# Optimization experiments

Measured on AMD Instinct MI355X. Metric: run time of the kernel, lower is better.

The kernel has to match this reference:

```python
import jax, jax.numpy as jnp
import numpy as np
import math


def hs_pe(x, fr, fi):
    # x: [N, c, h, w], c = cp*3; fr/fi: [max_len, cp] real/imag of freqs_cis.
    N, c, h, w = x.shape
    cp = c // 3
    xs = x.reshape(N, cp, 3, h, w)
    a, b, c3 = xs[:, :, 0], xs[:, :, 1], xs[:, :, 2]
    # rotate (a, b) as complex along h axis
    frh = fr[:h].T[None, :, :, None]  # [1, cp, h, 1]
    fih = fi[:h].T[None, :, :, None]
    a2 = a * frh - b * fih
    b2 = a * fih + b * frh
    # rotate (b2, c3) as complex along w axis
    frw = fr[:w].T[None, :, None, :]  # [1, cp, 1, w]
    fiw = fi[:w].T[None, :, None, :]
    b3 = b2 * frw - c3 * fiw
    c32 = b2 * fiw + c3 * frw
    return jnp.stack([a2, b3, c32], axis=2).reshape(N, c, h, w)


def partition(x, ws, dr):
    # OverlapDilatedWindowPartion
    B, C, H, W = x.shape
    Wsz = ws + dr
    st = Wsz // 2
    nh = math.ceil(H / Wsz)
    nw = math.ceil(W / Wsz)
    x = jnp.pad(x, ((0, 0), (0, 0), (0, nh * Wsz - H), (0, nw * Wsz - W)), mode='reflect')
    x = jnp.concatenate([x, jnp.pad(x[:, :, st:, :], ((0, 0), (0, 0), (0, st), (0, 0)), mode='reflect')], axis=0)
    x = jnp.concatenate([x, jnp.pad(x[:, :, :, st:], ((0, 0), (0, 0), (0, 0), (0, st)), mode='reflect')], axis=0)
    gb = x.shape[0]
    # 'gb c (nh h) (nw w) -> (nh nw gb) c h w'
    x = x.reshape(gb, C, nh, Wsz, nw, Wsz).transpose(2, 4, 0, 1, 3, 5).reshape(nh * nw * gb, C, Wsz, Wsz)
    return x[:, :, :ws, :ws]


def reverse(win, ws, dr, B, H, W):
    # OverlapDilatedWindowReverse
    Wsz = ws + dr
    st = Wsz // 2
    nh = math.ceil(H / Wsz)
    nw = math.ceil(W / Wsz)
    bH, bW = nh * Wsz, nw * Wsz
    win = jnp.pad(win, ((0, 0), (0, 0), (0, dr), (0, dr)))
    C = win.shape[1]
    # '(nh nw g b) c h w -> g b c (nh h) (nw w)'
    x = win.reshape(nh, nw, 4, B, C, Wsz, Wsz).transpose(2, 3, 4, 0, 5, 1, 6).reshape(4, B, C, bH, bW)
    x0 = x[0]
    x1 = jnp.pad(x[1], ((0, 0), (0, 0), (st, 0), (0, 0)))[:, :, :bH, :]
    x2 = jnp.pad(x[2], ((0, 0), (0, 0), (0, 0), (st, 0)))[:, :, :, :bW]
    x3 = jnp.pad(x[3], ((0, 0), (0, 0), (st, 0), (st, 0)))[:, :, :bH, :bW]
    return (x0 + x1 + x2 + x3)[:, :, :H, :W]


HEAD_NUM = 8
WINDOW_SIZE = 8
DILATE_RATE = 4


def setup_inputs() -> dict:
    key = jax.random.key(0)
    k1, k2, k3 = jax.random.split(key, 3)
    B, C, H, W = 1, 576, 192, 192
    x = jax.random.normal(k1, (B, C, H, W), dtype=jnp.float32)
    # rotary frequencies on the unit circle: [window_size, d//3, 2] (real, imag)
    theta = jax.random.uniform(k2, (WINDOW_SIZE, C // (3 * HEAD_NUM) // 3), dtype=jnp.float32) * (2 * np.pi)
    freqs_cis = jnp.stack([jnp.cos(theta), jnp.sin(theta)], axis=-1)
    weight = jax.random.uniform(k3, (1, 1, H, W), dtype=jnp.float32, minval=0.5, maxval=1.5)
    return {"x": x, "freqs_cis": freqs_cis, "weight": weight}


def reference(x, freqs_cis, weight):
    B, C, H, W = x.shape
    ws, dr, n = WINDOW_SIZE, DILATE_RATE, HEAD_NUM
    win = partition(x, ws, dr)  # [Nw, C, ws, ws]
    Nw = win.shape[0]
    d = C // (3 * n)
    # '(k n d)' channel split, k outer, d fastest
    qkv = win.reshape(Nw, 3, n, d, ws, ws).transpose(1, 0, 2, 3, 4, 5).reshape(3, Nw * n, d, ws, ws)
    fr, fi = freqs_cis[..., 0], freqs_cis[..., 1]
    q = hs_pe(qkv[0], fr, fi)
    k = hs_pe(qkv[1], fr, fi)
    v = qkv[2]
    def toseq(t):
        return t.reshape(Nw * n, d, ws * ws).transpose(0, 2, 1)  # [Nw*n, L, d]
    q, k, v = toseq(q), toseq(k), toseq(v)
    scale = jnp.sqrt(jnp.asarray(d, q.dtype))
    attn = jax.nn.softmax(jnp.einsum('nld,nmd->nlm', q, k) / scale, axis=-1)
    out = jnp.einsum('nlm,nmd->nld', attn, v)
    # '(Nw n) (h w) d -> Nw (n d) h w'
    out = out.reshape(Nw, n, ws, ws, d).transpose(0, 1, 4, 2, 3).reshape(Nw, n * d, ws, ws)
    out = reverse(out, ws, dr, B, H, W)
    return out / weight
```

## Files before the change

### kernel.cpp

```cpp
#include <hip/hip_runtime.h>

#define HW 36864
#define HDIM 192
#define NUNITS 8192
#define UPB 2
#define UDW 2688
#define QO 0
#define KO 768
#define VTO 1536
#define PO 0
#define O_BYTES (8192ull * 768 * 4)
#define Y_BYTES (8ull * HW * 72 * 2)

typedef __fp16 h2  __attribute__((ext_vector_type(2)));
typedef __fp16 v8h __attribute__((ext_vector_type(8)));
typedef float  v4f __attribute__((ext_vector_type(4)));

static __device__ __forceinline__ h2 pk2(float a, float b) {
    return __builtin_amdgcn_cvt_pkrtz(a, b);
}
static __device__ __forceinline__ unsigned h2u(h2 x) {
    union { h2 h; unsigned u; } c; c.h = x; return c.u;
}
static __device__ __forceinline__ h2 u2h(unsigned x) {
    union { unsigned u; h2 h; } c; c.u = x; return c.h;
}
static __device__ __forceinline__ v8h as_v8h(uint4 u) {
    union { uint4 u; v8h h; } c; c.u = u; return c.h;
}

__global__ __launch_bounds__(256)
void transpose_x(const float* __restrict__ x, uint4* __restrict__ y4) {
    const int idx  = blockIdx.x * 256 + threadIdx.x;
    const int head = idx / HW;
    const int pix  = idx - head * HW;
    const float* xp = x + (size_t)(head * 24) * HW + pix;

    unsigned o[36];
#pragma unroll
    for (int qkv = 0; qkv < 3; ++qkv)
#pragma unroll
        for (int dp = 0; dp < 12; ++dp) {
            const float a = xp[(size_t)(qkv * 192 + 2 * dp)     * HW];
            const float b = xp[(size_t)(qkv * 192 + 2 * dp + 1) * HW];
            o[qkv * 12 + dp] = h2u(pk2(a, b));
        }
    uint4* dst = y4 + (size_t)head * 9 * HW + pix;
#pragma unroll
    for (int j = 0; j < 9; ++j) dst[(size_t)j * HW] = *(const uint4*)&o[4 * j];
}

__global__ __launch_bounds__(128, 4)
void attn_mfma(const float* __restrict__ x,
               const uint4* __restrict__ y4,
               const float* __restrict__ fc,
               const float* __restrict__ wgt,
               float* __restrict__ out,
               unsigned* __restrict__ wsO)
{
    __shared__ unsigned lds[UPB * UDW];
    __shared__ float frs[64], fis[64];
    __shared__ unsigned zblk[4];

    const int wave = threadIdx.x >> 6;
    const int lane = threadIdx.x & 63;
    const int gid  = blockIdx.x * UPB + wave;
    const int head = gid & 7;
    const int wi   = gid >> 3;
    const int g    = wi & 3;
    const int iw   = (wi >> 2) & 15;
    const int ih   = wi >> 6;

    unsigned* uld = &lds[wave * UDW];

    if (threadIdx.x < 64) {
        float2 t = ((const float2*)fc)[threadIdx.x];
        frs[threadIdx.x] = t.x; fis[threadIdx.x] = t.y;
    } else if (threadIdx.x < 68) {
        zblk[threadIdx.x - 64] = 0;
    }
    __syncthreads();

    const int r = lane >> 3, col = lane & 7;
    const int h0 = ih * 12 + r, w0 = iw * 12 + col;
    int in_h = h0 + ((g & 1) ? 6 : 0); if (in_h >= HDIM) in_h = 2 * HDIM - 2 - in_h;
    int in_w = w0 + ((g & 2) ? 6 : 0); if (in_w >= HDIM) in_w = 2 * HDIM - 2 - in_w;

    float q[24], k[24], v[24];
    if (y4) {
        const uint4* yb = y4 + (size_t)head * 9 * HW + (size_t)in_h * HDIM + in_w;
        uint4 qa = yb[0],        qb = yb[(size_t)HW],     qc = yb[(size_t)2 * HW];
        uint4 ka = yb[(size_t)3 * HW], kb = yb[(size_t)4 * HW], kc = yb[(size_t)5 * HW];
        uint4 va = yb[(size_t)6 * HW], vb = yb[(size_t)7 * HW], vc = yb[(size_t)8 * HW];
#pragma unroll
        for (int j = 0; j < 4; ++j) {
            h2 t;
            t = u2h(((const unsigned*)&qa)[j]); q[2*j]    = (float)t[0]; q[2*j+1]    = (float)t[1];
            t = u2h(((const unsigned*)&qb)[j]); q[8+2*j]  = (float)t[0]; q[8+2*j+1]  = (float)t[1];
            t = u2h(((const unsigned*)&qc)[j]); q[16+2*j] = (float)t[0]; q[16+2*j+1] = (float)t[1];
            t = u2h(((const unsigned*)&ka)[j]); k[2*j]    = (float)t[0]; k[2*j+1]    = (float)t[1];
            t = u2h(((const unsigned*)&kb)[j]); k[8+2*j]  = (float)t[0]; k[8+2*j+1]  = (float)t[1];
            t = u2h(((const unsigned*)&kc)[j]); k[16+2*j] = (float)t[0]; k[16+2*j+1] = (float)t[1];
            t = u2h(((const unsigned*)&va)[j]); v[2*j]    = (float)t[0]; v[2*j+1]    = (float)t[1];
            t = u2h(((const unsigned*)&vb)[j]); v[8+2*j]  = (float)t[0]; v[8+2*j+1]  = (float)t[1];
            t = u2h(((const unsigned*)&vc)[j]); v[16+2*j] = (float)t[0]; v[16+2*j+1] = (float)t[1];
        }
    } else {
        const float* xb = x + (size_t)(head * 24) * HW + in_h * HDIM + in_w;
#pragma unroll
        for (int dd = 0; dd < 24; ++dd) q[dd] = xb[(size_t)dd * HW];
#pragma unroll
        for (int dd = 0; dd < 24; ++dd) k[dd] = xb[(size_t)dd * HW + (size_t)192 * HW];
#pragma unroll
        for (int dd = 0; dd < 24; ++dd) v[dd] = xb[(size_t)dd * HW + (size_t)384 * HW];
    }

#pragma unroll
    for (int p = 0; p < 8; ++p) {
        const float frr = frs[r * 8 + p],   fir = fis[r * 8 + p];
        const float frc = frs[col * 8 + p], fic = fis[col * 8 + p];
        {
            float a = q[3*p], b = q[3*p+1], c3 = q[3*p+2];
            float b2 = a * fir + b * frr;
            q[3*p]   = a * frr - b * fir;
            q[3*p+1] = b2 * frc - c3 * fic;
            q[3*p+2] = b2 * fic + c3 * frc;
        }
        {
            float a = k[3*p], b = k[3*p+1], c3 = k[3*p+2];
            float b2 = a * fir + b * frr;
            k[3*p]   = a * frr - b * fir;
            k[3*p+1] = b2 * frc - c3 * fic;
            k[3*p+2] = b2 * fic + c3 * frc;
        }
    }

    {
        const float sc = 0.29448903f;
        uint2* qw = (uint2*)&uld[QO + lane * 12];
        uint2* kw = (uint2*)&uld[KO + lane * 12];
#pragma unroll
        for (int j = 0; j < 3; ++j) {
            qw[2*j]   = make_uint2(h2u(pk2(q[8*j]*sc,   q[8*j+1]*sc)),
                                   h2u(pk2(q[8*j+2]*sc, q[8*j+3]*sc)));
            qw[2*j+1] = make_uint2(h2u(pk2(q[8*j+4]*sc, q[8*j+5]*sc)),
                                   h2u(pk2(q[8*j+6]*sc, q[8*j+7]*sc)));
            kw[2*j]   = make_uint2(h2u(pk2(k[8*j],   k[8*j+1])),
                                   h2u(pk2(k[8*j+2], k[8*j+3])));
            kw[2*j+1] = make_uint2(h2u(pk2(k[8*j+4], k[8*j+5])),
                                   h2u(pk2(k[8*j+6], k[8*j+7])));
        }
    }
    {
#pragma unroll
        for (int i = 0; i < 5; ++i) {
            int idx = lane + i * 64;
            if (idx < 288) uld[VTO + 24 * 36 + idx] = 0;
        }
        __fp16* vt = (__fp16*)&uld[VTO];
        vt[24 * 72 + lane] = (__fp16)1.0f;
#pragma unroll
        for (int dd = 0; dd < 24; ++dd) vt[dd * 72 + lane] = (__fp16)v[dd];
    }
    asm volatile("" ::: "memory");

    const int qq = lane >> 4, l15 = lane & 15;
    v8h Qf[4], Kf[4];
#pragma unroll
    for (int t = 0; t < 4; ++t) {
        const unsigned* qa = (qq < 3) ? &uld[QO + (16*t + l15)*12 + 4*qq] : zblk;
        const unsigned* ka = (qq < 3) ? &uld[KO + (16*t + l15)*12 + 4*qq] : zblk;
        Qf[t] = as_v8h(*(const uint4*)qa);
        Kf[t] = as_v8h(*(const uint4*)ka);
    }
    v8h Vf[2][2];
#pragma unroll
    for (int dt = 0; dt < 2; ++dt)
#pragma unroll
        for (int ks = 0; ks < 2; ++ks)
            Vf[dt][ks] = as_v8h(*(const uint4*)&uld[VTO + (16*dt + l15)*36 + 16*ks + 4*qq]);

#pragma unroll
    for (int tn = 0; tn < 4; ++tn) {
#pragma unroll
        for (int tm = 0; tm < 4; ++tm) {
            v4f c = {0.f, 0.f, 0.f, 0.f};
            c = __builtin_amdgcn_mfma_f32_16x16x32_f16(Kf[tn], Qf[tm], c, 0, 0, 0);
            uint2 w = make_uint2(h2u(pk2(__builtin_amdgcn_exp2f(c[0]),
                                         __builtin_amdgcn_exp2f(c[1]))),
                                 h2u(pk2(__builtin_amdgcn_exp2f(c[2]),
                                         __builtin_amdgcn_exp2f(c[3]))));
            *(uint2*)&uld[PO + (16*tm + l15)*36 + 8*tn + 2*qq] = w;
        }
    }

    v4f O[2][4];
#pragma unroll
    for (int dt = 0; dt < 2; ++dt)
#pragma unroll
        for (int lt = 0; lt < 4; ++lt)
            O[dt][lt] = (v4f){0.f, 0.f, 0.f, 0.f};
#pragma unroll
    for (int lt = 0; lt < 4; ++lt) {
#pragma unroll
        for (int ks = 0; ks < 2; ++ks) {
            v8h Pf = as_v8h(*(const uint4*)&uld[PO + (16*lt + l15)*36 + 16*ks + 4*qq]);
            O[0][lt] = __builtin_amdgcn_mfma_f32_16x16x32_f16(Vf[0][ks], Pf, O[0][lt], 0, 0, 0);
            O[1][lt] = __builtin_amdgcn_mfma_f32_16x16x32_f16(Vf[1][ks], Pf, O[1][lt], 0, 0, 0);
        }
    }

    float inv[4];
#pragma unroll
    for (int lt = 0; lt < 4; ++lt)
        inv[lt] = 1.0f / __shfl(O[1][lt][0], 32 + l15, 64);

    if (wsO) {
        unsigned* wb = wsO + (size_t)gid * 768;
#pragma unroll
        for (int lt = 0; lt < 4; ++lt) {
            const int   l  = 16*lt + l15;
            const float sc = inv[lt];
            wb[(2*qq+0) * 64 + l] = h2u(pk2(O[0][lt][0]*sc, O[0][lt][1]*sc));
            wb[(2*qq+1) * 64 + l] = h2u(pk2(O[0][lt][2]*sc, O[0][lt][3]*sc));
            if (qq < 2) {
                wb[(8+2*qq)   * 64 + l] = h2u(pk2(O[1][lt][0]*sc, O[1][lt][1]*sc));
                wb[(8+2*qq+1) * 64 + l] = h2u(pk2(O[1][lt][2]*sc, O[1][lt][3]*sc));
            }
        }
    } else {
#pragma unroll
        for (int lt = 0; lt < 4; ++lt) {
            const int l  = 16*lt + l15;
            const int oh = ih * 12 + (l >> 3) + ((g & 1) ? 6 : 0);
            const int ow = iw * 12 + (l & 7)  + ((g & 2) ? 6 : 0);
            if (oh < HDIM && ow < HDIM) {
                const float sc = inv[lt] / wgt[oh * HDIM + ow];
                float* ob = out + (size_t)(head * 24) * HW + oh * HDIM + ow;
#pragma unroll
                for (int rg = 0; rg < 4; ++rg)
                    atomicAdd(ob + (size_t)(4*qq + rg) * HW, O[0][lt][rg] * sc);
                if (qq < 2) {
#pragma unroll
                    for (int rg = 0; rg < 4; ++rg)
                        atomicAdd(ob + (size_t)(16 + 4*qq + rg) * HW, O[1][lt][rg] * sc);
                }
            }
        }
    }
}

__global__ __launch_bounds__(256)
void merge_out(const unsigned* __restrict__ wsO,
               const float* __restrict__ wgt,
               float* __restrict__ out)
{
    const int idx = blockIdx.x * 256 + threadIdx.x;
    const int p   = idx / HW;
    const int pix = idx - p * HW;
    const int h   = pix / HDIM;
    const int w   = pix - h * HDIM;
    const int head = p / 12;
    const int dp   = p - head * 12;

    float a0 = 0.f, a1 = 0.f;
#pragma unroll
    for (int g = 0; g < 4; ++g) {
        const int hh = h - ((g & 1) ? 6 : 0);
        const int ww = w - ((g & 2) ? 6 : 0);
        if (hh < 0 || ww < 0) continue;
        const int ih = hh / 12, r  = hh - ih * 12;
        const int iw = ww / 12, cw = ww - iw * 12;
        if (r >= 8 || cw >= 8) continue;
        const int unit = ((ih * 16 + iw) * 4 + g) * 8 + head;
        const h2 t = u2h(wsO[(size_t)unit * 768 + dp * 64 + r * 8 + cw]);
        a0 += (float)t[0];
        a1 += (float)t[1];
    }
    const float wv = wgt[pix];
    const size_t c0 = (size_t)(head * 24 + 2 * dp) * HW + pix;
    out[c0]      = a0 / wv;
    out[c0 + HW] = a1 / wv;
}

extern "C" void kernel_launch(void* const* d_in, const int* in_sizes, int n_in,
                              void* d_out, int out_size, void* d_ws, size_t ws_size,
                              hipStream_t stream) {
    const float* x   = (const float*)d_in[0];
    const float* fc  = (const float*)d_in[1];
    const float* wgt = (const float*)d_in[2];
    float* out = (float*)d_out;

    unsigned* wsO = ws_size >= O_BYTES ? (unsigned*)d_ws : nullptr;

    if (!wsO)
        (void)hipMemsetAsync(out, 0, (size_t)out_size * sizeof(float), stream);
    attn_mfma<<<NUNITS / UPB, UPB * 64, 0, stream>>>(x, nullptr, fc, wgt, out, wsO);
    if (wsO)
        merge_out<<<96 * HW / 256, 256, 0, stream>>>(wsO, wgt, out);
}
```

Before: 174.0 us.

## Store per-group attention outputs in image layout and vectorize merge

The attention kernel now writes fp16 window outputs straight into a per-group, per-channel-pair image-shaped workspace indexed by output pixel, replacing the old per-unit window layout. The merge kernel then reads contiguous pixel pairs with 8-byte loads and uses precomputed validity masks instead of per-group division to locate window entries, producing two pixels per thread with float2 stores. This is meant to make merge reads coalesced and cut index arithmetic. It also removes the unused transpose_x kernel and relaxes launch bounds from 4 to 2 blocks per SM, which allows more registers per thread at some cost in occupancy.

```diff
diff --git a/kernel.cpp b/kernel.cpp
--- a/kernel.cpp
+++ b/kernel.cpp
@@ -9,8 +9,7 @@
 #define KO 768
 #define VTO 1536
 #define PO 0
-#define O_BYTES (8192ull * 768 * 4)
-#define Y_BYTES (8ull * HW * 72 * 2)
+#define P_BYTES (384ull * HW * 4)
 
 typedef __fp16 h2  __attribute__((ext_vector_type(2)));
 typedef __fp16 v8h __attribute__((ext_vector_type(8)));
@@ -29,34 +28,12 @@
     union { uint4 u; v8h h; } c; c.u = u; return c.h;
 }
 
-__global__ __launch_bounds__(256)
-void transpose_x(const float* __restrict__ x, uint4* __restrict__ y4) {
-    const int idx  = blockIdx.x * 256 + threadIdx.x;
-    const int head = idx / HW;
-    const int pix  = idx - head * HW;
-    const float* xp = x + (size_t)(head * 24) * HW + pix;
-
-    unsigned o[36];
-#pragma unroll
-    for (int qkv = 0; qkv < 3; ++qkv)
-#pragma unroll
-        for (int dp = 0; dp < 12; ++dp) {
-            const float a = xp[(size_t)(qkv * 192 + 2 * dp)     * HW];
-            const float b = xp[(size_t)(qkv * 192 + 2 * dp + 1) * HW];
-            o[qkv * 12 + dp] = h2u(pk2(a, b));
-        }
-    uint4* dst = y4 + (size_t)head * 9 * HW + pix;
-#pragma unroll
-    for (int j = 0; j < 9; ++j) dst[(size_t)j * HW] = *(const uint4*)&o[4 * j];
-}
-
-__global__ __launch_bounds__(128, 4)
+__global__ __launch_bounds__(128, 2)
 void attn_mfma(const float* __restrict__ x,
-               const uint4* __restrict__ y4,
                const float* __restrict__ fc,
                const float* __restrict__ wgt,
                float* __restrict__ out,
-               unsigned* __restrict__ wsO)
+               unsigned* __restrict__ wsP)
 {
     __shared__ unsigned lds[UPB * UDW];
     __shared__ float frs[64], fis[64];
@@ -87,25 +64,7 @@
     int in_w = w0 + ((g & 2) ? 6 : 0); if (in_w >= HDIM) in_w = 2 * HDIM - 2 - in_w;
 
     float q[24], k[24], v[24];
-    if (y4) {
-        const uint4* yb = y4 + (size_t)head * 9 * HW + (size_t)in_h * HDIM + in_w;
-        uint4 qa = yb[0],        qb = yb[(size_t)HW],     qc = yb[(size_t)2 * HW];
-        uint4 ka = yb[(size_t)3 * HW], kb = yb[(size_t)4 * HW], kc = yb[(size_t)5 * HW];
-        uint4 va = yb[(size_t)6 * HW], vb = yb[(size_t)7 * HW], vc = yb[(size_t)8 * HW];
-#pragma unroll
-        for (int j = 0; j < 4; ++j) {
-            h2 t;
-            t = u2h(((const unsigned*)&qa)[j]); q[2*j]    = (float)t[0]; q[2*j+1]    = (float)t[1];
-            t = u2h(((const unsigned*)&qb)[j]); q[8+2*j]  = (float)t[0]; q[8+2*j+1]  = (float)t[1];
-            t = u2h(((const unsigned*)&qc)[j]); q[16+2*j] = (float)t[0]; q[16+2*j+1] = (float)t[1];
-            t = u2h(((const unsigned*)&ka)[j]); k[2*j]    = (float)t[0]; k[2*j+1]    = (float)t[1];
-            t = u2h(((const unsigned*)&kb)[j]); k[8+2*j]  = (float)t[0]; k[8+2*j+1]  = (float)t[1];
-            t = u2h(((const unsigned*)&kc)[j]); k[16+2*j] = (float)t[0]; k[16+2*j+1] = (float)t[1];
-            t = u2h(((const unsigned*)&va)[j]); v[2*j]    = (float)t[0]; v[2*j+1]    = (float)t[1];
-            t = u2h(((const unsigned*)&vb)[j]); v[8+2*j]  = (float)t[0]; v[8+2*j+1]  = (float)t[1];
-            t = u2h(((const unsigned*)&vc)[j]); v[16+2*j] = (float)t[0]; v[16+2*j+1] = (float)t[1];
-        }
-    } else {
+    {
         const float* xb = x + (size_t)(head * 24) * HW + in_h * HDIM + in_w;
 #pragma unroll
         for (int dd = 0; dd < 24; ++dd) q[dd] = xb[(size_t)dd * HW];
@@ -215,17 +174,23 @@
     for (int lt = 0; lt < 4; ++lt)
         inv[lt] = 1.0f / __shfl(O[1][lt][0], 32 + l15, 64);
 
-    if (wsO) {
-        unsigned* wb = wsO + (size_t)gid * 768;
+    if (wsP) {
+        const int goffh = (g & 1) ? 6 : 0, goffw = (g & 2) ? 6 : 0;
+        unsigned* pb = wsP + (size_t)((g * 8 + head) * 12) * HW;
 #pragma unroll
         for (int lt = 0; lt < 4; ++lt) {
-            const int   l  = 16*lt + l15;
-            const float sc = inv[lt];
-            wb[(2*qq+0) * 64 + l] = h2u(pk2(O[0][lt][0]*sc, O[0][lt][1]*sc));
-            wb[(2*qq+1) * 64 + l] = h2u(pk2(O[0][lt][2]*sc, O[0][lt][3]*sc));
-            if (qq < 2) {
-                wb[(8+2*qq)   * 64 + l] = h2u(pk2(O[1][lt][0]*sc, O[1][lt][1]*sc));
-                wb[(8+2*qq+1) * 64 + l] = h2u(pk2(O[1][lt][2]*sc, O[1][lt][3]*sc));
+            const int l  = 16*lt + l15;
+            const int oh = ih * 12 + (l >> 3) + goffh;
+            const int ow = iw * 12 + (l & 7)  + goffw;
+            if (oh < HDIM && ow < HDIM) {
+                const float  sc = inv[lt];
+                const size_t o  = (size_t)oh * HDIM + ow;
+                pb[(size_t)(2*qq+0) * HW + o] = h2u(pk2(O[0][lt][0]*sc, O[0][lt][1]*sc));
+                pb[(size_t)(2*qq+1) * HW + o] = h2u(pk2(O[0][lt][2]*sc, O[0][lt][3]*sc));
+                if (qq < 2) {
+                    pb[(size_t)(8+2*qq) * HW + o] = h2u(pk2(O[1][lt][0]*sc, O[1][lt][1]*sc));
+                    pb[(size_t)(9+2*qq) * HW + o] = h2u(pk2(O[1][lt][2]*sc, O[1][lt][3]*sc));
+                }
             }
         }
     } else {
@@ -251,36 +216,49 @@
 }
 
 __global__ __launch_bounds__(256)
-void merge_out(const unsigned* __restrict__ wsO,
+void merge_out(const unsigned* __restrict__ wsP,
                const float* __restrict__ wgt,
                float* __restrict__ out)
 {
     const int idx = blockIdx.x * 256 + threadIdx.x;
-    const int p   = idx / HW;
-    const int pix = idx - p * HW;
-    const int h   = pix / HDIM;
+    const int pp  = idx / (HW / 2);
+    const int px2 = idx - pp * (HW / 2);
+    const int pix = 2 * px2;
+    const int h   = px2 / (HDIM / 2);
     const int w   = pix - h * HDIM;
-    const int head = p / 12;
-    const int dp   = p - head * 12;
-
-    float a0 = 0.f, a1 = 0.f;
+    const int head = pp / 12;
+    const int dp   = pp - head * 12;
+
+    const int hm = h % 12;
+    const bool vh0 = hm < 8;
+    int hm6 = hm + 6; if (hm6 >= 12) hm6 -= 12;
+    const bool vh1 = (h >= 6) && (hm6 < 8);
+
+    const int wm = w % 12;
+    const bool vw0a = wm < 8;
+    const int wmb = (wm == 11) ? 0 : wm + 1;
+    const bool vw0b = wmb < 8;
+    int wm6 = wm + 6; if (wm6 >= 12) wm6 -= 12;
+    const bool vw1a = (w >= 6) && (wm6 < 8);
+    const int wm6b = (wm6 == 11) ? 0 : wm6 + 1;
+    const bool vw1b = (w + 1 >= 6) && (wm6b < 8);
+
+    float a0 = 0.f, a1 = 0.f, b0 = 0.f, b1 = 0.f;
 #pragma unroll
     for (int g = 0; g < 4; ++g) {
-        const int hh = h - ((g & 1) ? 6 : 0);
-        const int ww = w - ((g & 2) ? 6 : 0);
-        if (hh < 0 || ww < 0) continue;
-        const int ih = hh / 12, r  = hh - ih * 12;
-        const int iw = ww / 12, cw = ww - iw * 12;
-        if (r >= 8 || cw >= 8) continue;
-        const int unit = ((ih * 16 + iw) * 4 + g) * 8 + head;
-        const h2 t = u2h(wsO[(size_t)unit * 768 + dp * 64 + r * 8 + cw]);
-        a0 += (float)t[0];
-        a1 += (float)t[1];
-    }
-    const float wv = wgt[pix];
+        const bool vh = (g & 1) ? vh1 : vh0;
+        const bool va = vh && ((g & 2) ? vw1a : vw0a);
+        const bool vb = vh && ((g & 2) ? vw1b : vw0b);
+        if (va || vb) {
+            const uint2 u = *(const uint2*)&wsP[(size_t)(g * 96 + pp) * HW + pix];
+            if (va) { h2 t = u2h(u.x); a0 += (float)t[0]; a1 += (float)t[1]; }
+            if (vb) { h2 t = u2h(u.y); b0 += (float)t[0]; b1 += (float)t[1]; }
+        }
+    }
+    const float2 wv = *(const float2*)&wgt[pix];
     const size_t c0 = (size_t)(head * 24 + 2 * dp) * HW + pix;
-    out[c0]      = a0 / wv;
-    out[c0 + HW] = a1 / wv;
+    *(float2*)&out[c0]      = make_float2(a0 / wv.x, b0 / wv.y);
+    *(float2*)&out[c0 + HW] = make_float2(a1 / wv.x, b1 / wv.y);
 }
 
 extern "C" void kernel_launch(void* const* d_in, const int* in_sizes, int n_in,
@@ -291,11 +269,11 @@
     const float* wgt = (const float*)d_in[2];
     float* out = (float*)d_out;
 
-    unsigned* wsO = ws_size >= O_BYTES ? (unsigned*)d_ws : nullptr;
-
-    if (!wsO)
+    unsigned* wsP = ws_size >= P_BYTES ? (unsigned*)d_ws : nullptr;
+
+    if (!wsP)
         (void)hipMemsetAsync(out, 0, (size_t)out_size * sizeof(float), stream);
-    attn_mfma<<<NUNITS / UPB, UPB * 64, 0, stream>>>(x, nullptr, fc, wgt, out, wsO);
-    if (wsO)
-        merge_out<<<96 * HW / 256, 256, 0, stream>>>(wsO, wgt, out);
-}
+    attn_mfma<<<NUNITS / UPB, UPB * 64, 0, stream>>>(x, fc, wgt, out, wsP);
+    if (wsP)
+        merge_out<<<96 * (HW / 2) / 256, 256, 0, stream>>>(wsP, wgt, out);
+}
```

Result: slower. 181.7 us (+4.4%).
